# Performance work log

Measured on AMD Instinct MI355X. Metric: run time of the kernel, lower is better.

The kernel has to match this reference:

```python
import jax, jax.numpy as jnp
import numpy as np

LEAKY_SLOPE = 0.05        # self.alpha is overwritten to 0.05 in __init__
NEG_INF = -9.0e15         # masking constant from the source
THRESH = 0.5              # connection_threshold

B, N, F = 8, 2048, 128


def setup_inputs() -> dict:
    key = jax.random.key(0)
    k1, k2, k3, k4, k5 = jax.random.split(key, 5)
    h = jax.random.normal(k1, (B, N, F), dtype=jnp.float32)
    W = jax.random.normal(k2, (F, F), dtype=jnp.float32) * (1.414 / np.sqrt(F))
    a = jax.random.normal(k3, (2 * F, 1), dtype=jnp.float32) * 0.1
    A1 = jax.random.normal(k4, (4 * N, N), dtype=jnp.float32) * (1.414 / np.sqrt(N))
    A2 = jax.random.normal(k5, (N, 4 * N), dtype=jnp.float32) * (1.414 / np.sqrt(4 * N))
    return {"h": h, "W": W, "a": a, "A1": A1, "A2": A2}


def reference(h, W, a, A1, A2):
    f = W.shape[0]
    # Wh = h @ W^T  (torch Linear stores weight as [out, in])
    Wh = jnp.einsum('bnf,gf->bng', h, W)                       # [B,N,F]
    # additive GAT scores: e[b,i,j] = leaky_relu(Wh_i.a1 + Wh_j.a2)
    Wh1 = Wh @ a[:f, :]                                        # [B,N,1]
    Wh2 = Wh @ a[f:, :]                                        # [B,N,1]
    e = Wh1 + jnp.swapaxes(Wh2, 1, 2)                          # [B,N,N]
    e = jnp.where(e > 0, e, LEAKY_SLOPE * e)                   # LeakyReLU(0.05)
    # learned adjacency gate over last dim (computed in the original forward
    # but never used for the returned output -> dead code; kept for fidelity)
    hid = jax.nn.sigmoid(jnp.einsum('bij,hj->bih', e, A1))     # [B,N,4N]
    adj = jax.nn.sigmoid(e + jnp.einsum('bih,jh->bij', hid, A2))
    adj = jnp.where(adj > THRESH, adj, 0.0)                    # unused downstream
    # masked softmax attention over e itself
    attention = jax.nn.softmax(jnp.where(e > 0, e, NEG_INF), axis=2)
    # dropout is identity in eval mode (training=False)
    h_prime = jnp.einsum('bij,bjf->bif', attention, Wh)        # [B,N,F]
    return jax.nn.elu(h_prime)                                 # concat=True branch
```

## Files before the change

### kernel.cpp

```cpp
#include <hip/hip_runtime.h>
#include <math.h>

#define BB 8
#define NN 2048
#define FF 128
#define CH 128
#define CHSZ 16

typedef __attribute__((ext_vector_type(8))) short short8;
typedef __attribute__((ext_vector_type(4))) float f32x4;

__device__ __forceinline__ ushort f2bf(float x) {
    uint u = __float_as_uint(x);
    uint r = (u + 0x7FFFu + ((u >> 16) & 1u)) >> 16;
    return (ushort)r;
}
__device__ __forceinline__ float bf2f(ushort x) {
    return __uint_as_float(((uint)x) << 16);
}


__global__ __launch_bounds__(256) void k1_wh(
        const float* __restrict__ h, const float* __restrict__ W,
        const float* __restrict__ a, float* __restrict__ Wh,
        float* __restrict__ s1, float* __restrict__ s2) {
    __shared__ __align__(16) ushort Whi[128][136];
    __shared__ __align__(16) ushort Wlo[128][136];
    __shared__ __align__(16) ushort hhi[64][136];
    __shared__ __align__(16) ushort hlo[64][136];
    const int tid = threadIdx.x;
    const int blk = blockIdx.x;
    const int bb = blk & 7;
    const int w8 = blk >> 3;
    const int row0 = (bb * 32 + w8) * 64;

    for (int i = tid; i < 4096; i += 256) {
        int g = i >> 5, k4 = (i & 31) * 4;
        float4 wv = *(const float4*)&W[g * 128 + k4];
        ushort h0 = f2bf(wv.x), h1 = f2bf(wv.y), h2 = f2bf(wv.z), h3 = f2bf(wv.w);
        ushort l0 = f2bf(wv.x - bf2f(h0)), l1 = f2bf(wv.y - bf2f(h1));
        ushort l2 = f2bf(wv.z - bf2f(h2)), l3 = f2bf(wv.w - bf2f(h3));
        uint2 hw, lw;
        hw.x = (uint)h0 | ((uint)h1 << 16); hw.y = (uint)h2 | ((uint)h3 << 16);
        lw.x = (uint)l0 | ((uint)l1 << 16); lw.y = (uint)l2 | ((uint)l3 << 16);
        *(uint2*)&Whi[g][k4] = hw;
        *(uint2*)&Wlo[g][k4] = lw;
    }
    for (int i = tid; i < 2048; i += 256) {
        int r = i >> 5, k4 = (i & 31) * 4;
        float4 hv = *(const float4*)&h[(row0 + r) * 128 + k4];
        ushort h0 = f2bf(hv.x), h1 = f2bf(hv.y), h2 = f2bf(hv.z), h3 = f2bf(hv.w);
        ushort l0 = f2bf(hv.x - bf2f(h0)), l1 = f2bf(hv.y - bf2f(h1));
        ushort l2 = f2bf(hv.z - bf2f(h2)), l3 = f2bf(hv.w - bf2f(h3));
        uint2 hw, lw;
        hw.x = (uint)h0 | ((uint)h1 << 16); hw.y = (uint)h2 | ((uint)h3 << 16);
        lw.x = (uint)l0 | ((uint)l1 << 16); lw.y = (uint)l2 | ((uint)l3 << 16);
        *(uint2*)&hhi[r][k4] = hw;
        *(uint2*)&hlo[r][k4] = lw;
    }
    __syncthreads();

    const int lane = tid & 63;
    const int wid = tid >> 6;
    const int gl = lane & 15;
    const int kg = lane >> 4;
    const int lr = wid * 16 + gl;

    f32x4 acc[8];
#pragma unroll
    for (int gt = 0; gt < 8; ++gt) acc[gt] = (f32x4){0.f, 0.f, 0.f, 0.f};

#pragma unroll
    for (int t = 0; t < 4; ++t) {
        const int k0 = t * 32 + kg * 8;
        short8 ah = *(const short8*)&hhi[lr][k0];
        short8 al = *(const short8*)&hlo[lr][k0];
#pragma unroll
        for (int gt = 0; gt < 8; ++gt) {
            const int g = gt * 16 + gl;
            short8 bh = *(const short8*)&Whi[g][k0];
            short8 bl = *(const short8*)&Wlo[g][k0];
            acc[gt] = __builtin_amdgcn_mfma_f32_16x16x32_bf16(ah, bh, acc[gt], 0, 0, 0);
            acc[gt] = __builtin_amdgcn_mfma_f32_16x16x32_bf16(ah, bl, acc[gt], 0, 0, 0);
            acc[gt] = __builtin_amdgcn_mfma_f32_16x16x32_bf16(al, bh, acc[gt], 0, 0, 0);
        }
    }

    float p1a[4] = {0.f, 0.f, 0.f, 0.f}, p2a[4] = {0.f, 0.f, 0.f, 0.f};
#pragma unroll
    for (int gt = 0; gt < 8; ++gt) {
        const int g = gt * 16 + gl;
        const float a1v = a[g];
        const float a2v = a[128 + g];
#pragma unroll
        for (int r = 0; r < 4; ++r) {
            float wvv = acc[gt][r];
            Wh[(row0 + wid * 16 + kg * 4 + r) * 128 + g] = wvv;
            p1a[r] += wvv * a1v;
            p2a[r] += wvv * a2v;
        }
    }
#pragma unroll
    for (int s = 1; s < 16; s <<= 1) {
#pragma unroll
        for (int r = 0; r < 4; ++r) {
            p1a[r] += __shfl_xor(p1a[r], s, 64);
            p2a[r] += __shfl_xor(p2a[r], s, 64);
        }
    }
    if (gl == 0) {
#pragma unroll
        for (int r = 0; r < 4; ++r) {
            int row = row0 + wid * 16 + kg * 4 + r;
            s1[row] = p1a[r];
            s2[row] = p2a[r];
        }
    }
}

__global__ __launch_bounds__(512) void k2_rank(
        const float* __restrict__ s2, const float* __restrict__ s1,
        int* __restrict__ idxs, float* __restrict__ ps,
        int* __restrict__ lo_arr) {
    __shared__ __align__(16) float ls[NN];
    __shared__ int part[8][64];
    __shared__ int lpart[8][64];
    __shared__ float wmax[8];
    const int t = threadIdx.x;
    const int blk = blockIdx.x;
    const int b = blk & 7;
    const int seg = blk >> 3;
    const int base = b * NN;
    float4* ls4 = (float4*)ls;
    const float4* g4 = (const float4*)(s2 + base);
    float m;
    {
        float4 v4 = g4[t];
        ls4[t] = v4;
        m = fmaxf(fmaxf(v4.x, v4.y), fmaxf(v4.z, v4.w));
    }
#pragma unroll
    for (int s = 1; s < 64; s <<= 1) m = fmaxf(m, __shfl_xor(m, s, 64));
    if ((t & 63) == 0) wmax[t >> 6] = m;
    __syncthreads();
    float M = wmax[0];
#pragma unroll
    for (int i = 1; i < 8; ++i) M = fmaxf(M, wmax[i]);
    const int jj = t & 63;
    const int w  = t >> 6;
    const int j  = seg * 64 + jj;
    const float v = ls[j];
    const float s1v = s1[base + j];
    int rank = 0, cnt = 0;
#pragma unroll 8
    for (int q = 0; q < 64; ++q) {
        float4 kv = ls4[w * 64 + q];
        int kg = w * 256 + q * 4;
        rank += (kv.x < v) | ((kv.x == v) & (kg + 0 < j));
        rank += (kv.y < v) | ((kv.y == v) & (kg + 1 < j));
        rank += (kv.z < v) | ((kv.z == v) & (kg + 2 < j));
        rank += (kv.w < v) | ((kv.w == v) & (kg + 3 < j));
        cnt += (s1v + kv.x <= 0.f);
        cnt += (s1v + kv.y <= 0.f);
        cnt += (s1v + kv.z <= 0.f);
        cnt += (s1v + kv.w <= 0.f);
    }
    part[w][jj] = rank;
    lpart[w][jj] = cnt;
    __syncthreads();
    if (t < 64) {
        int r = 0, lo = 0;
#pragma unroll
        for (int ww = 0; ww < 8; ++ww) {
            r  += part[ww][t];
            lo += lpart[ww][t];
        }
        int jg = seg * 64 + t;
        float vv = ls[jg];
        idxs[base + r] = jg;
        ps[base + r] = expf(vv - M);
        lo_arr[base + jg] = lo;
    }
}

__global__ __launch_bounds__(512) void k34(
        const float* __restrict__ Wh, const int* __restrict__ idxs,
        const float* __restrict__ ps, const int* __restrict__ lo_arr,
        float* __restrict__ out) {
    __shared__ __align__(16) float cs[CH][132];
    __shared__ float lp[CH];
    __shared__ float mvp[8][128];
    __shared__ float mv[128];
    __shared__ float segt[4][128];
    __shared__ __align__(16) int   lidx[NN];
    __shared__ __align__(16) float lps[NN];
    const int tid = threadIdx.x;
    const int blk = blockIdx.x;
    const int b = blk & 7;
    const int seg = blk >> 3;
    const int base = b * NN;

    *(int4*)&lidx[tid * 4]  = ((const int4*)(idxs + base))[tid];
    *(float4*)&lps[tid * 4] = ((const float4*)(ps + base))[tid];
    __syncthreads();

    {
        const int lane = tid & 63;
        const int w = tid >> 6;
        const int f2 = lane * 2;
        float ux = 0.f, uy = 0.f;
#pragma unroll 2
        for (int cc = 0; cc < 16; ++cc) {
            const int c = w * 16 + cc;
            float ax = 0.f, ay = 0.f, pacc = 0.f;
#pragma unroll
            for (int t = CHSZ - 1; t >= 0; --t) {
                const int r = c * CHSZ + t;
                const int j = lidx[r];
                const float pv = lps[r];
                float2 wv = *(const float2*)&Wh[(base + j) * 128 + f2];
                ax += pv * wv.x;
                ay += pv * wv.y;
                ux += wv.x;
                uy += wv.y;
                pacc += pv;
            }
            cs[c][f2] = ax;
            cs[c][f2 + 1] = ay;
            if (lane == 0) lp[c] = pacc;
        }
        mvp[w][f2] = ux;
        mvp[w][f2 + 1] = uy;
    }
    __syncthreads();

    const int q = tid >> 7;
    const int f = tid & 127;
    float suf[32];
    {
        float acc = 0.f;
#pragma unroll
        for (int i = 31; i >= 0; --i) {
            acc += cs[q * 32 + i][f];
            suf[i] = acc;
        }
        segt[q][f] = acc;
    }
    if (tid < 64) {
        float p0 = lp[tid * 2];
        float p1v = lp[tid * 2 + 1];
        float T = p0 + p1v;
#pragma unroll
        for (int s = 1; s < 64; s <<= 1) {
            float t2 = __shfl_down(T, s, 64);
            if (tid + s < 64) T += t2;
        }
        float E = __shfl_down(T, 1, 64);
        if (tid == 63) E = 0.f;
        lp[tid * 2]     = p0 + p1v + E;
        lp[tid * 2 + 1] = p1v + E;
    }
    if (tid < 128) {
        float s = 0.f;
#pragma unroll
        for (int ww = 0; ww < 8; ++ww) s += mvp[ww][tid];
        mv[tid] = s * (1.f / (float)NN);
    }
    __syncthreads();
    {
        float off = 0.f;
#pragma unroll
        for (int qq = 1; qq < 4; ++qq)
            if (q + qq < 4) off += segt[q + qq][f];
#pragma unroll
        for (int i = 0; i < 32; ++i)
            cs[q * 32 + i][f] = suf[i] + off;
    }
    __syncthreads();

#pragma unroll
    for (int pass = 0; pass < 4; ++pass) {
        const int rowg = base + seg * 64 + pass * 16 + (tid >> 5);
        const int fq = (tid & 31) * 4;
        const int lo = lo_arr[rowg];
        float4 v;
        if (lo == NN) {
            v = make_float4(mv[fq], mv[fq + 1], mv[fq + 2], mv[fq + 3]);
        } else {
            const int c = lo >> 4;
            float4 pp = make_float4(0.f, 0.f, 0.f, 0.f);
            float den_p = 0.f;
            for (int r = c * CHSZ + CHSZ - 1; r >= lo; --r) {
                const int j = lidx[r];
                const float pv = lps[r];
                float4 wv = *(const float4*)&Wh[(base + j) * 128 + fq];
                pp.x += pv * wv.x;
                pp.y += pv * wv.y;
                pp.z += pv * wv.z;
                pp.w += pv * wv.w;
                den_p += pv;
            }
            float4 csv = make_float4(0.f, 0.f, 0.f, 0.f);
            float lpE = 0.f;
            if (c < CH - 1) {
                csv = *(const float4*)&cs[c + 1][fq];
                lpE = lp[c + 1];
            }
            const float den = den_p + lpE;
            v.x = (pp.x + csv.x) / den;
            v.y = (pp.y + csv.y) / den;
            v.z = (pp.z + csv.z) / den;
            v.w = (pp.w + csv.w) / den;
        }
        v.x = (v.x > 0.f) ? v.x : expm1f(v.x);
        v.y = (v.y > 0.f) ? v.y : expm1f(v.y);
        v.z = (v.z > 0.f) ? v.z : expm1f(v.z);
        v.w = (v.w > 0.f) ? v.w : expm1f(v.w);
        *(float4*)&out[rowg * 128 + fq] = v;
    }
}

extern "C" void kernel_launch(void* const* d_in, const int* in_sizes, int n_in,
                              void* d_out, int out_size, void* d_ws, size_t ws_size,
                              hipStream_t stream) {
    (void)in_sizes; (void)n_in; (void)out_size; (void)ws_size;
    const float* h = (const float*)d_in[0];
    const float* W = (const float*)d_in[1];
    const float* a = (const float*)d_in[2];
    float* out = (float*)d_out;

    float* Wh     = (float*)d_ws;
    float* s1     = Wh + 2097152;
    float* s2     = s1 + 16384;
    float* ps     = s2 + 16384;
    int*   idxs   = (int*)(ps + 16384);
    int*   lo_arr = idxs + 16384;

    k1_wh<<<BB * NN / 64, 256, 0, stream>>>(h, W, a, Wh, s1, s2);
    k2_rank<<<BB * 32, 512, 0, stream>>>(s2, s1, idxs, ps, lo_arr);
    k34<<<BB * 32, 512, 0, stream>>>(Wh, idxs, ps, lo_arr, out);
}
```

Measured before the change: 184.9 us.

## Split chunk partial sums into separate kernel to remove redundant per-block gather

Before, each of the 32 segment blocks per batch recomputed all 128 chunk partial sums by gathering the whole sorted Wh (2048 rows) for its batch. That repeated the same gather 32 times. A new kernel k3c computes each chunk's weighted sum, plain sum and probability sum once and writes them to workspace. The final kernel then only loads these precomputed partials. This adds an extra launch and a global round trip of roughly 1 MB of partials.

```diff
diff --git a/kernel.cpp b/kernel.cpp
--- a/kernel.cpp
+++ b/kernel.cpp
@@ -183,13 +183,41 @@
     }
 }
 
-__global__ __launch_bounds__(512) void k34(
+__global__ __launch_bounds__(128) void k3c(
         const float* __restrict__ Wh, const int* __restrict__ idxs,
-        const float* __restrict__ ps, const int* __restrict__ lo_arr,
+        const float* __restrict__ ps,
+        float* __restrict__ chunktot, float* __restrict__ chunku,
+        float* __restrict__ chunkp) {
+    const int blk = blockIdx.x;
+    const int b = blk & 7;
+    const int c = blk >> 3;
+    const int base = b * NN;
+    const int f = threadIdx.x;
+    float acc = 0.f, accu = 0.f, pacc = 0.f;
+#pragma unroll
+    for (int tt = CHSZ - 1; tt >= 0; --tt) {
+        int r = c * CHSZ + tt;
+        int jj = idxs[base + r];
+        float pv = ps[base + r];
+        float w = Wh[(base + jj) * 128 + f];
+        acc += pv * w;
+        accu += w;
+        pacc += pv;
+    }
+    chunktot[(b * CH + c) * 128 + f] = acc;
+    chunku[(b * CH + c) * 128 + f] = accu;
+    if (f == 0) chunkp[b * CH + c] = pacc;
+}
+
+__global__ __launch_bounds__(512) void k4f(
+        const float* __restrict__ chunktot, const float* __restrict__ chunku,
+        const float* __restrict__ chunkp,
+        const int* __restrict__ idxs, const float* __restrict__ ps,
+        const int* __restrict__ lo_arr, const float* __restrict__ Wh,
         float* __restrict__ out) {
     __shared__ __align__(16) float cs[CH][132];
     __shared__ float lp[CH];
-    __shared__ float mvp[8][128];
+    __shared__ float mvp[4][128];
     __shared__ float mv[128];
     __shared__ float segt[4][128];
     __shared__ __align__(16) int   lidx[NN];
@@ -202,37 +230,24 @@
 
     *(int4*)&lidx[tid * 4]  = ((const int4*)(idxs + base))[tid];
     *(float4*)&lps[tid * 4] = ((const float4*)(ps + base))[tid];
-    __syncthreads();
 
     {
-        const int lane = tid & 63;
-        const int w = tid >> 6;
-        const int f2 = lane * 2;
-        float ux = 0.f, uy = 0.f;
-#pragma unroll 2
-        for (int cc = 0; cc < 16; ++cc) {
-            const int c = w * 16 + cc;
-            float ax = 0.f, ay = 0.f, pacc = 0.f;
-#pragma unroll
-            for (int t = CHSZ - 1; t >= 0; --t) {
-                const int r = c * CHSZ + t;
-                const int j = lidx[r];
-                const float pv = lps[r];
-                float2 wv = *(const float2*)&Wh[(base + j) * 128 + f2];
-                ax += pv * wv.x;
-                ay += pv * wv.y;
-                ux += wv.x;
-                uy += wv.y;
-                pacc += pv;
-            }
-            cs[c][f2] = ax;
-            cs[c][f2 + 1] = ay;
-            if (lane == 0) lp[c] = pacc;
-        }
-        mvp[w][f2] = ux;
-        mvp[w][f2 + 1] = uy;
-    }
-    __syncthreads();
+        const int f  = tid & 127;
+        const int r0 = tid >> 7;
+        float su = 0.f;
+#pragma unroll 4
+        for (int i = 0; i < 32; ++i) {
+            int c = r0 + i * 4;
+            cs[c][f] = chunktot[(b * CH + c) * 128 + f];
+            su += chunku[(b * CH + c) * 128 + f];
+        }
+        mvp[r0][f] = su;
+        if (tid < CH) lp[tid] = chunkp[b * CH + tid];
+    }
+    __syncthreads();
+    if (tid < 128)
+        mv[tid] = (mvp[0][tid] + mvp[1][tid] + mvp[2][tid] + mvp[3][tid])
+                  * (1.f / (float)NN);
 
     const int q = tid >> 7;
     const int f = tid & 127;
@@ -259,12 +274,6 @@
         if (tid == 63) E = 0.f;
         lp[tid * 2]     = p0 + p1v + E;
         lp[tid * 2 + 1] = p1v + E;
-    }
-    if (tid < 128) {
-        float s = 0.f;
-#pragma unroll
-        for (int ww = 0; ww < 8; ++ww) s += mvp[ww][tid];
-        mv[tid] = s * (1.f / (float)NN);
     }
     __syncthreads();
     {
@@ -329,14 +338,19 @@
     const float* a = (const float*)d_in[2];
     float* out = (float*)d_out;
 
-    float* Wh     = (float*)d_ws;
-    float* s1     = Wh + 2097152;
-    float* s2     = s1 + 16384;
-    float* ps     = s2 + 16384;
-    int*   idxs   = (int*)(ps + 16384);
-    int*   lo_arr = idxs + 16384;
+    float* Wh       = (float*)d_ws;
+    float* s1       = Wh + 2097152;
+    float* s2       = s1 + 16384;
+    float* ps       = s2 + 16384;
+    int*   idxs     = (int*)(ps + 16384);
+    int*   lo_arr   = idxs + 16384;
+    float* chunktot = (float*)(lo_arr + 16384);
+    float* chunku   = chunktot + 131072;
+    float* chunkp   = chunku + 131072;
 
     k1_wh<<<BB * NN / 64, 256, 0, stream>>>(h, W, a, Wh, s1, s2);
     k2_rank<<<BB * 32, 512, 0, stream>>>(s2, s1, idxs, ps, lo_arr);
-    k34<<<BB * 32, 512, 0, stream>>>(Wh, idxs, ps, lo_arr, out);
-}
+    k3c<<<BB * CH, 128, 0, stream>>>(Wh, idxs, ps, chunktot, chunku, chunkp);
+    k4f<<<BB * 32, 512, 0, stream>>>(chunktot, chunku, chunkp,
+                                     idxs, ps, lo_arr, Wh, out);
+}
```

After: 176.5 us. 4.6% less time.
